# Performance work log

Hardware: AMD Instinct MI355X
Metric: run time of the kernel (lower is better)

## Reference

```python
import jax, jax.numpy as jnp
import numpy as np

D, NH = 1024, 16
B, L = 2, 2048
NEG = -1e9


def setup_inputs() -> dict:
    key = jax.random.key(0)
    ks = jax.random.split(key, 6)
    x = jax.random.normal(ks[0], (B, L, D), dtype=jnp.float32)
    # causal additive mask, broadcast over batch and heads
    causal = jnp.tril(jnp.ones((L, L), dtype=jnp.float32))
    mask = jnp.where(causal == 1.0, 0.0, NEG)[None, None, :, :]
    wx_w = jax.random.normal(ks[1], (3 * D, D), dtype=jnp.float32) * 0.02
    wx_b = jnp.zeros((3 * D,), dtype=jnp.float32)
    wo_w = jax.random.normal(ks[2], (D, D), dtype=jnp.float32) * 0.02
    wo_b = jnp.zeros((D,), dtype=jnp.float32)
    ln_g = jnp.ones((D,), dtype=jnp.float32)
    ln_b = jnp.zeros((D,), dtype=jnp.float32)
    return {"x": x, "mask": mask, "wx_w": wx_w, "wx_b": wx_b,
            "wo_w": wo_w, "wo_b": wo_b, "ln_g": ln_g, "ln_b": ln_b}


def _layernorm(x, g, b, eps=1e-5):
    mu = jnp.mean(x, axis=-1, keepdims=True)
    var = jnp.mean((x - mu) ** 2, axis=-1, keepdims=True)
    return (x - mu) * jax.lax.rsqrt(var + eps) * g + b


def reference(x, mask, wx_w, wx_b, wo_w, wo_b, ln_g, ln_b):
    b, l, d = x.shape
    nh = NH
    dh = d // nh
    h = _layernorm(x, ln_g, ln_b)
    proj = h @ wx_w.T + wx_b                       # [b, l, 3d]
    # 'b l (n nh dh) -> n b nh l dh'
    proj = proj.reshape(b, l, 3, nh, dh)
    q, k, v = jnp.moveaxis(proj, 2, 0).transpose(0, 1, 3, 2, 4)  # each [b, nh, l, dh]
    qkT = jnp.einsum('bhic,bhjc->bhij', q, k) + mask
    scale = jnp.asarray(d, jnp.float32) ** 0.5     # NOTE: sqrt(d), not sqrt(dh)
    attn = jax.nn.softmax(qkT / scale, axis=-1)
    heads = jnp.einsum('bhij,bhjc->bhic', attn, v)  # [b, nh, l, dh]
    heads = heads.transpose(0, 2, 1, 3).reshape(b, l, d)
    attention = heads @ wo_w.T + wo_b
    out = jax.nn.gelu(x + attention, approximate=False)
    return (out, mask)
```

## Files before the change

kernel.cpp:

```cpp
#include <hip/hip_runtime.h>
#include <hip/hip_bf16.h>
#include <math.h>

constexpr int kD  = 1024;
constexpr int kB  = 2;
constexpr int kL  = 2048;
constexpr int kM  = kB * kL;

typedef __attribute__((ext_vector_type(8))) short  bf8v;
typedef __attribute__((ext_vector_type(4))) float  f4v;
typedef __attribute__((ext_vector_type(4))) unsigned short us4v;

#define MFMA_BF16 __builtin_amdgcn_mfma_f32_16x16x32_bf16

__device__ inline unsigned short f2bf(float f) {
    __hip_bfloat16 h = __float2bfloat16(f);
    return *(unsigned short*)&h;
}
__device__ inline float bf2f(unsigned short u) {
    __hip_bfloat16 h = *(__hip_bfloat16*)&u;
    return __bfloat162float(h);
}
__device__ inline void gload16(const void* g, void* l) {
    __builtin_amdgcn_global_load_lds(
        (const __attribute__((address_space(1))) void*)g,
        (__attribute__((address_space(3))) void*)l, 16, 0, 0);
}

__global__ __launch_bounds__(256) void convert_split(
    const float* __restrict__ src, unsigned short* __restrict__ hi,
    unsigned short* __restrict__ lo, int n4)
{
    const int i = blockIdx.x * 256 + threadIdx.x;
    if (i >= n4) return;
    const float4 v = ((const float4*)src)[i];
    const float vv[4] = {v.x, v.y, v.z, v.w};
    us4v h, l;
    #pragma unroll
    for (int c = 0; c < 4; ++c) {
        h[c] = f2bf(vv[c]);
        l[c] = f2bf(vv[c] - bf2f(h[c]));
    }
    *(us4v*)&hi[(size_t)i * 4] = h;
    *(us4v*)&lo[(size_t)i * 4] = l;
}

__global__ __launch_bounds__(256) void ln_kernel(
    const float* __restrict__ x, const float* __restrict__ g,
    const float* __restrict__ beta, unsigned short* __restrict__ h_hi)
{
    const int row = blockIdx.x;
    const int tid = threadIdx.x;
    const float4 v = ((const float4*)(x + (size_t)row * kD))[tid];
    float s  = v.x + v.y + v.z + v.w;
    float s2 = v.x*v.x + v.y*v.y + v.z*v.z + v.w*v.w;
    #pragma unroll
    for (int off = 32; off > 0; off >>= 1) {
        s  += __shfl_down(s, off);
        s2 += __shfl_down(s2, off);
    }
    __shared__ float wsum[4], wsum2[4];
    const int lane = tid & 63, wid = tid >> 6;
    if (lane == 0) { wsum[wid] = s; wsum2[wid] = s2; }
    __syncthreads();
    const float ts   = wsum[0] + wsum[1] + wsum[2] + wsum[3];
    const float ts2  = wsum2[0] + wsum2[1] + wsum2[2] + wsum2[3];
    const float mean = ts * (1.0f / kD);
    const float var  = ts2 * (1.0f / kD) - mean * mean;
    const float rstd = rsqrtf(var + 1e-5f);
    const float4 gv = ((const float4*)g)[tid];
    const float4 bv = ((const float4*)beta)[tid];
    float o[4];
    o[0] = (v.x - mean) * rstd * gv.x + bv.x;
    o[1] = (v.y - mean) * rstd * gv.y + bv.y;
    o[2] = (v.z - mean) * rstd * gv.z + bv.z;
    o[3] = (v.w - mean) * rstd * gv.w + bv.w;
    us4v h;
    #pragma unroll
    for (int c = 0; c < 4; ++c) h[c] = f2bf(o[c]);
    *(us4v*)&h_hi[(size_t)row * kD + tid * 4] = h;
}

template<int MODE>
__global__ __launch_bounds__(256, 3) void gemm_split(
    const unsigned short* __restrict__ A,
    const unsigned short* __restrict__ Bhi, const unsigned short* __restrict__ Blo,
    const float* __restrict__ bias, const float* __restrict__ resid,
    unsigned short* __restrict__ outb, unsigned short* __restrict__ vT,
    float* __restrict__ outf, int N, int K)
{
    __shared__ unsigned short S[3][128][32];
    const int tid = threadIdx.x;
    const int l = tid & 63, w = tid >> 6;
    const int col16 = l & 15, grp = l >> 4;
    const int wr = (w >> 1) * 64, wc = (w & 1) * 64;
    const int row0 = blockIdx.y * 128, col0 = blockIdx.x * 128;
    const int sr = l >> 2;
    const int sc8 = ((l & 3) ^ ((sr >> 1) & 3)) * 8;
    const unsigned short* gb = (w == 0) ? A : (w == 1) ? Bhi : Blo;
    const int rb = (w == 0) ? row0 : col0;
    const int pos8 = (grp ^ ((col16 >> 1) & 3)) * 8;
    f4v acc[4][4] = {};

    for (int k0 = 0; k0 < K; k0 += 32) {
        __syncthreads();
        if (w < 3) {
            #pragma unroll
            for (int t = 0; t < 8; ++t)
                gload16(gb + (size_t)(rb + t*16 + sr) * K + k0 + sc8,
                        &S[w][t*16][0]);
        }
        __syncthreads();
        bf8v ah[4];
        #pragma unroll
        for (int mi = 0; mi < 4; ++mi)
            ah[mi] = *(bf8v*)&S[0][wr + mi*16 + col16][pos8];
        #pragma unroll
        for (int ni = 0; ni < 4; ++ni) {
            const bf8v bh = *(bf8v*)&S[1][wc + ni*16 + col16][pos8];
            const bf8v bl = *(bf8v*)&S[2][wc + ni*16 + col16][pos8];
            #pragma unroll
            for (int mi = 0; mi < 4; ++mi) {
                acc[mi][ni] = MFMA_BF16(ah[mi], bh, acc[mi][ni], 0, 0, 0);
                acc[mi][ni] = MFMA_BF16(ah[mi], bl, acc[mi][ni], 0, 0, 0);
            }
        }
    }
    #pragma unroll
    for (int mi = 0; mi < 4; ++mi)
        #pragma unroll
        for (int ni = 0; ni < 4; ++ni) {
            const int gcol = col0 + wc + ni*16 + col16;
            const float bb = bias[gcol];
            #pragma unroll
            for (int rr = 0; rr < 4; ++rr) {
                const int grow = row0 + wr + mi*16 + grp*4 + rr;
                float o = acc[mi][ni][rr] + bb;
                if (MODE == 0) {
                    if (gcol < 2048) {
                        if (gcol < 1024) o *= (1.0f / 32.0f);
                        outb[(size_t)grow * 3072 + gcol] = f2bf(o);
                    } else {
                        const int dg = gcol - 2048;
                        vT[((size_t)((grow >> 11) * 16 + (dg >> 6)) * 64 + (dg & 63)) * 2048
                           + (grow & 2047)] = f2bf(o);
                    }
                } else {
                    o += resid[(size_t)grow * N + gcol];
                    o = 0.5f * o * (1.0f + erff(o * 0.70710678118654752f));
                    outf[(size_t)grow * N + gcol] = o;
                }
            }
        }
}

__global__ __launch_bounds__(256, 4) void attn_mfma(
    const unsigned short* __restrict__ projb, const unsigned short* __restrict__ vT,
    unsigned short* __restrict__ heads_hi)
{
    __shared__ unsigned short Ks[64 * 64];
    __shared__ unsigned short Vs[64 * 64];
    __shared__ unsigned int   Ps32[4][16][68];
    const int tid = threadIdx.x;
    const int l = tid & 63, w = tid >> 6;
    const int col16 = l & 15, grp = l >> 4;
    const int bh = blockIdx.x, b = bh >> 4, hh = bh & 15;
    const int qt = 31 - (int)blockIdx.y;
    const int q0 = qt * 64;
    const unsigned short* vTh = vT + (size_t)bh * 64 * 2048;

    const int r8 = l >> 3;
    const int sc8 = ((l & 7) ^ r8) * 8;
    const int isV = w >> 1;
    const int t0 = (w & 1) * 4;
    const int sw7 = col16 & 7;

    const size_t qbase = (size_t)(b*kL + q0 + w*16 + col16) * 3072 + hh*64 + grp*8;
    bf8v aq[2];
    aq[0] = *(const bf8v*)&projb[qbase];
    aq[1] = *(const bf8v*)&projb[qbase + 32];

    f4v accO[4] = {};
    float m_r[4], l_r[4];
    #pragma unroll
    for (int r = 0; r < 4; ++r) { m_r[r] = -INFINITY; l_r[r] = 0.0f; }

    for (int jt = 0; jt <= qt; ++jt) {
        const int j0 = jt * 64;
        __syncthreads();
        #pragma unroll
        for (int t2 = 0; t2 < 4; ++t2) {
            const int t = t0 + t2;
            if (isV)
                gload16(&vTh[(size_t)(t*8 + r8) * 2048 + j0 + sc8], &Vs[t*8*64]);
            else
                gload16(&projb[(size_t)(b*kL + j0 + t*8 + r8) * 3072 + hh*64 + 1024 + sc8],
                        &Ks[t*8*64]);
        }
        __syncthreads();

        f4v accS[4] = {};
        #pragma unroll
        for (int kk = 0; kk < 2; ++kk)
            #pragma unroll
            for (int nj = 0; nj < 4; ++nj) {
                const int row = nj*16 + col16;
                const bf8v bk = *(bf8v*)&Ks[row*64 + (((grp + kk*4) ^ sw7) * 8)];
                accS[nj] = MFMA_BF16(aq[kk], bk, accS[nj], 0, 0, 0);
            }

        const bool diag = (jt == qt);
        float p[4][4];
        float alpha[4];
        #pragma unroll
        for (int r = 0; r < 4; ++r) {
            const int q_local = w*16 + grp*4 + r;
            float sv[4];
            #pragma unroll
            for (int nj = 0; nj < 4; ++nj) {
                sv[nj] = accS[nj][r];
                if (diag && (nj*16 + col16 > q_local)) sv[nj] = -1e9f;
            }
            float pm = fmaxf(fmaxf(sv[0], sv[1]), fmaxf(sv[2], sv[3]));
            pm = fmaxf(pm, __shfl_xor(pm, 1));
            pm = fmaxf(pm, __shfl_xor(pm, 2));
            pm = fmaxf(pm, __shfl_xor(pm, 4));
            pm = fmaxf(pm, __shfl_xor(pm, 8));
            const float m_new = fmaxf(m_r[r], pm);
            alpha[r] = __expf(m_r[r] - m_new);
            m_r[r] = m_new;
            float ps = 0.0f;
            #pragma unroll
            for (int nj = 0; nj < 4; ++nj) {
                p[nj][r] = __expf(sv[nj] - m_new);
                ps += p[nj][r];
            }
            ps += __shfl_xor(ps, 1);
            ps += __shfl_xor(ps, 2);
            ps += __shfl_xor(ps, 4);
            ps += __shfl_xor(ps, 8);
            l_r[r] = l_r[r] * alpha[r] + ps;
        }
        #pragma unroll
        for (int nd = 0; nd < 4; ++nd)
            #pragma unroll
            for (int r = 0; r < 4; ++r)
                accO[nd][r] *= alpha[r];

        #pragma unroll
        for (int nj = 0; nj < 4; ++nj)
            #pragma unroll
            for (int r = 0; r < 4; ++r) {
                const unsigned hi = f2bf(p[nj][r]);
                const unsigned lo = f2bf(p[nj][r] - bf2f((unsigned short)hi));
                Ps32[w][grp*4 + r][nj*16 + col16] = hi | (lo << 16);
            }
        asm volatile("s_waitcnt lgkmcnt(0)" ::: "memory");

        #pragma unroll
        for (int js = 0; js < 2; ++js) {
            const uint4 pa0 = *(const uint4*)&Ps32[w][col16][js*32 + grp*8];
            const uint4 pa1 = *(const uint4*)&Ps32[w][col16][js*32 + grp*8 + 4];
            const unsigned pu[8] = {pa0.x, pa0.y, pa0.z, pa0.w,
                                    pa1.x, pa1.y, pa1.z, pa1.w};
            bf8v ph, pl;
            #pragma unroll
            for (int i = 0; i < 8; ++i) {
                ph[i] = (short)(pu[i] & 0xffffu);
                pl[i] = (short)(pu[i] >> 16);
            }
            #pragma unroll
            for (int nd = 0; nd < 4; ++nd) {
                const int row = nd*16 + col16;
                const bf8v bv = *(bf8v*)&Vs[row*64 + (((grp + js*4) ^ sw7) * 8)];
                accO[nd] = MFMA_BF16(ph, bv, accO[nd], 0, 0, 0);
                accO[nd] = MFMA_BF16(pl, bv, accO[nd], 0, 0, 0);
            }
        }
    }
    #pragma unroll
    for (int nd = 0; nd < 4; ++nd)
        #pragma unroll
        for (int r = 0; r < 4; ++r) {
            const float o = accO[nd][r] / l_r[r];
            heads_hi[(size_t)(b*kL + q0 + w*16 + grp*4 + r) * kD
                     + hh*64 + nd*16 + col16] = f2bf(o);
        }
}

extern "C" void kernel_launch(void* const* d_in, const int* in_sizes, int n_in,
                              void* d_out, int out_size, void* d_ws, size_t ws_size,
                              hipStream_t stream)
{
    const float* x    = (const float*)d_in[0];
    const float* mask = (const float*)d_in[1];
    const float* wx_w = (const float*)d_in[2];
    const float* wx_b = (const float*)d_in[3];
    const float* wo_w = (const float*)d_in[4];
    const float* wo_b = (const float*)d_in[5];
    const float* ln_g = (const float*)d_in[6];
    const float* ln_b = (const float*)d_in[7];
    float* out = (float*)d_out;

    unsigned short* h_hi  = (unsigned short*)d_ws;
    unsigned short* h_lo  = h_hi  + (size_t)kM * kD;
    unsigned short* wxhi  = h_lo  + (size_t)kM * kD;
    unsigned short* wxlo  = wxhi  + (size_t)3 * kD * kD;
    unsigned short* wohi  = wxlo  + (size_t)3 * kD * kD;
    unsigned short* wolo  = wohi  + (size_t)kD * kD;
    unsigned short* projb = wolo  + (size_t)kD * kD;
    unsigned short* hd_hi = projb + (size_t)kM * 3 * kD;
    unsigned short* vT    = hd_hi + (size_t)kM * kD;

    convert_split<<<(3*kD*kD/4 + 255)/256, 256, 0, stream>>>(wx_w, wxhi, wxlo, 3*kD*kD/4);
    convert_split<<<(kD*kD/4 + 255)/256, 256, 0, stream>>>(wo_w, wohi, wolo, kD*kD/4);
    ln_kernel<<<kM, 256, 0, stream>>>(x, ln_g, ln_b, h_hi);
    gemm_split<0><<<dim3(3*kD/128, kM/128), 256, 0, stream>>>(
        h_hi, wxhi, wxlo, wx_b, nullptr, projb, vT, nullptr, 3*kD, kD);
    attn_mfma<<<dim3(kB*16, kL/64), 256, 0, stream>>>(projb, vT, hd_hi);
    gemm_split<1><<<dim3(kD/128, kM/128), 256, 0, stream>>>(
        hd_hi, wohi, wolo, wo_b, x, nullptr, nullptr, out, kD, kD);
    hipMemcpyAsync(out + (size_t)kM * kD, mask, (size_t)kL * kL * sizeof(float),
                   hipMemcpyDeviceToDevice, stream);
}
```

Measured before the change: 294.7 us.

## Double-buffer GEMM and attention LDS tiles, drop P lo split, skip rescale

Both the GEMM and the attention kernel now double-buffer their shared-memory tiles and prefetch the next K-step or key tile while computing on the current one, which removes one barrier per iteration and overlaps the global-to-LDS loads with MFMA work. The attention kernel also stops splitting P into hi/lo bf16 parts, halving the P·V MFMAs, which costs precision in the probabilities. It skips the online-softmax rescale of the accumulator when no row maximum grows anywhere in the wave. The extra LDS lowers the attention occupancy hint from 4 to 3 blocks.

```diff
diff --git a/kernel.cpp b/kernel.cpp
--- a/kernel.cpp
+++ b/kernel.cpp
@@ -89,7 +89,7 @@
     unsigned short* __restrict__ outb, unsigned short* __restrict__ vT,
     float* __restrict__ outf, int N, int K)
 {
-    __shared__ unsigned short S[3][128][32];
+    __shared__ unsigned short S[2][3][128][32];
     const int tid = threadIdx.x;
     const int l = tid & 63, w = tid >> 6;
     const int col16 = l & 15, grp = l >> 4;
@@ -102,29 +102,32 @@
     const int pos8 = (grp ^ ((col16 >> 1) & 3)) * 8;
     f4v acc[4][4] = {};
 
+    auto stage = [&](int buf, int k0s) {
+        #pragma unroll
+        for (int t = 0; t < 8; ++t)
+            gload16(gb + (size_t)(rb + t*16 + sr) * K + k0s + sc8,
+                    &S[buf][w][t*16][0]);
+    };
+    if (w < 3) stage(0, 0);
+    int cur = 0;
     for (int k0 = 0; k0 < K; k0 += 32) {
         __syncthreads();
-        if (w < 3) {
-            #pragma unroll
-            for (int t = 0; t < 8; ++t)
-                gload16(gb + (size_t)(rb + t*16 + sr) * K + k0 + sc8,
-                        &S[w][t*16][0]);
-        }
-        __syncthreads();
+        if (w < 3 && k0 + 32 < K) stage(cur ^ 1, k0 + 32);
         bf8v ah[4];
         #pragma unroll
         for (int mi = 0; mi < 4; ++mi)
-            ah[mi] = *(bf8v*)&S[0][wr + mi*16 + col16][pos8];
+            ah[mi] = *(bf8v*)&S[cur][0][wr + mi*16 + col16][pos8];
         #pragma unroll
         for (int ni = 0; ni < 4; ++ni) {
-            const bf8v bh = *(bf8v*)&S[1][wc + ni*16 + col16][pos8];
-            const bf8v bl = *(bf8v*)&S[2][wc + ni*16 + col16][pos8];
+            const bf8v bh = *(bf8v*)&S[cur][1][wc + ni*16 + col16][pos8];
+            const bf8v bl = *(bf8v*)&S[cur][2][wc + ni*16 + col16][pos8];
             #pragma unroll
             for (int mi = 0; mi < 4; ++mi) {
                 acc[mi][ni] = MFMA_BF16(ah[mi], bh, acc[mi][ni], 0, 0, 0);
                 acc[mi][ni] = MFMA_BF16(ah[mi], bl, acc[mi][ni], 0, 0, 0);
             }
         }
+        cur ^= 1;
     }
     #pragma unroll
     for (int mi = 0; mi < 4; ++mi)
@@ -154,12 +157,12 @@
         }
 }
 
-__global__ __launch_bounds__(256, 4) void attn_mfma(
+__global__ __launch_bounds__(256, 3) void attn_mfma(
     const unsigned short* __restrict__ projb, const unsigned short* __restrict__ vT,
     unsigned short* __restrict__ heads_hi)
 {
-    __shared__ unsigned short Ks[64 * 64];
-    __shared__ unsigned short Vs[64 * 64];
+    __shared__ unsigned short Ks[2][64 * 64];
+    __shared__ unsigned short Vs[2][64 * 64];
     __shared__ unsigned int   Ps32[4][16][68];
     const int tid = threadIdx.x;
     const int l = tid & 63, w = tid >> 6;
@@ -185,19 +188,23 @@
     #pragma unroll
     for (int r = 0; r < 4; ++r) { m_r[r] = -INFINITY; l_r[r] = 0.0f; }
 
-    for (int jt = 0; jt <= qt; ++jt) {
-        const int j0 = jt * 64;
-        __syncthreads();
+    auto stage = [&](int buf, int j0s) {
         #pragma unroll
         for (int t2 = 0; t2 < 4; ++t2) {
             const int t = t0 + t2;
             if (isV)
-                gload16(&vTh[(size_t)(t*8 + r8) * 2048 + j0 + sc8], &Vs[t*8*64]);
+                gload16(&vTh[(size_t)(t*8 + r8) * 2048 + j0s + sc8],
+                        &Vs[buf][t*8*64]);
             else
-                gload16(&projb[(size_t)(b*kL + j0 + t*8 + r8) * 3072 + hh*64 + 1024 + sc8],
-                        &Ks[t*8*64]);
-        }
+                gload16(&projb[(size_t)(b*kL + j0s + t*8 + r8) * 3072 + hh*64 + 1024 + sc8],
+                        &Ks[buf][t*8*64]);
+        }
+    };
+    stage(0, 0);
+    int cur = 0;
+    for (int jt = 0; jt <= qt; ++jt) {
         __syncthreads();
+        if (jt < qt) stage(cur ^ 1, (jt + 1) * 64);
 
         f4v accS[4] = {};
         #pragma unroll
@@ -205,56 +212,60 @@
             #pragma unroll
             for (int nj = 0; nj < 4; ++nj) {
                 const int row = nj*16 + col16;
-                const bf8v bk = *(bf8v*)&Ks[row*64 + (((grp + kk*4) ^ sw7) * 8)];
+                const bf8v bk = *(bf8v*)&Ks[cur][row*64 + (((grp + kk*4) ^ sw7) * 8)];
                 accS[nj] = MFMA_BF16(aq[kk], bk, accS[nj], 0, 0, 0);
             }
 
         const bool diag = (jt == qt);
-        float p[4][4];
-        float alpha[4];
+        float sv[4][4], pm[4];
         #pragma unroll
         for (int r = 0; r < 4; ++r) {
             const int q_local = w*16 + grp*4 + r;
-            float sv[4];
             #pragma unroll
             for (int nj = 0; nj < 4; ++nj) {
-                sv[nj] = accS[nj][r];
-                if (diag && (nj*16 + col16 > q_local)) sv[nj] = -1e9f;
-            }
-            float pm = fmaxf(fmaxf(sv[0], sv[1]), fmaxf(sv[2], sv[3]));
-            pm = fmaxf(pm, __shfl_xor(pm, 1));
-            pm = fmaxf(pm, __shfl_xor(pm, 2));
-            pm = fmaxf(pm, __shfl_xor(pm, 4));
-            pm = fmaxf(pm, __shfl_xor(pm, 8));
-            const float m_new = fmaxf(m_r[r], pm);
-            alpha[r] = __expf(m_r[r] - m_new);
-            m_r[r] = m_new;
+                sv[r][nj] = accS[nj][r];
+                if (diag && (nj*16 + col16 > q_local)) sv[r][nj] = -1e9f;
+            }
+            float p = fmaxf(fmaxf(sv[r][0], sv[r][1]), fmaxf(sv[r][2], sv[r][3]));
+            p = fmaxf(p, __shfl_xor(p, 1));
+            p = fmaxf(p, __shfl_xor(p, 2));
+            p = fmaxf(p, __shfl_xor(p, 4));
+            p = fmaxf(p, __shfl_xor(p, 8));
+            pm[r] = p;
+        }
+        const bool grow = (pm[0] > m_r[0]) || (pm[1] > m_r[1]) ||
+                          (pm[2] > m_r[2]) || (pm[3] > m_r[3]);
+        if (__any(grow)) {
+            #pragma unroll
+            for (int r = 0; r < 4; ++r) {
+                const float m_new = fmaxf(m_r[r], pm[r]);
+                const float al = __expf(m_r[r] - m_new);
+                m_r[r] = m_new;
+                l_r[r] *= al;
+                #pragma unroll
+                for (int nd = 0; nd < 4; ++nd) accO[nd][r] *= al;
+            }
+        }
+        float p[4][4];
+        #pragma unroll
+        for (int r = 0; r < 4; ++r) {
             float ps = 0.0f;
             #pragma unroll
             for (int nj = 0; nj < 4; ++nj) {
-                p[nj][r] = __expf(sv[nj] - m_new);
+                p[nj][r] = __expf(sv[r][nj] - m_r[r]);
                 ps += p[nj][r];
             }
             ps += __shfl_xor(ps, 1);
             ps += __shfl_xor(ps, 2);
             ps += __shfl_xor(ps, 4);
             ps += __shfl_xor(ps, 8);
-            l_r[r] = l_r[r] * alpha[r] + ps;
-        }
-        #pragma unroll
-        for (int nd = 0; nd < 4; ++nd)
+            l_r[r] += ps;
+        }
+        #pragma unroll
+        for (int nj = 0; nj < 4; ++nj)
             #pragma unroll
             for (int r = 0; r < 4; ++r)
-                accO[nd][r] *= alpha[r];
-
-        #pragma unroll
-        for (int nj = 0; nj < 4; ++nj)
-            #pragma unroll
-            for (int r = 0; r < 4; ++r) {
-                const unsigned hi = f2bf(p[nj][r]);
-                const unsigned lo = f2bf(p[nj][r] - bf2f((unsigned short)hi));
-                Ps32[w][grp*4 + r][nj*16 + col16] = hi | (lo << 16);
-            }
+                Ps32[w][grp*4 + r][nj*16 + col16] = (unsigned)f2bf(p[nj][r]);
         asm volatile("s_waitcnt lgkmcnt(0)" ::: "memory");
 
         #pragma unroll
@@ -263,20 +274,17 @@
             const uint4 pa1 = *(const uint4*)&Ps32[w][col16][js*32 + grp*8 + 4];
             const unsigned pu[8] = {pa0.x, pa0.y, pa0.z, pa0.w,
                                     pa1.x, pa1.y, pa1.z, pa1.w};
-            bf8v ph, pl;
-            #pragma unroll
-            for (int i = 0; i < 8; ++i) {
-                ph[i] = (short)(pu[i] & 0xffffu);
-                pl[i] = (short)(pu[i] >> 16);
-            }
+            bf8v ph;
+            #pragma unroll
+            for (int i = 0; i < 8; ++i) ph[i] = (short)(pu[i] & 0xffffu);
             #pragma unroll
             for (int nd = 0; nd < 4; ++nd) {
                 const int row = nd*16 + col16;
-                const bf8v bv = *(bf8v*)&Vs[row*64 + (((grp + js*4) ^ sw7) * 8)];
+                const bf8v bv = *(bf8v*)&Vs[cur][row*64 + (((grp + js*4) ^ sw7) * 8)];
                 accO[nd] = MFMA_BF16(ph, bv, accO[nd], 0, 0, 0);
-                accO[nd] = MFMA_BF16(pl, bv, accO[nd], 0, 0, 0);
-            }
-        }
+            }
+        }
+        cur ^= 1;
     }
     #pragma unroll
     for (int nd = 0; nd < 4; ++nd)
```

New measurement: 277.1 us. -6.0%, faster.
